# Performance work log

Measured on AMD Instinct MI355X. Metric: run time of the kernel, lower is better.

The kernel has to match this reference:

```python
import jax, jax.numpy as jnp
import numpy as np

EPS = 1e-6
B, S, D = 2, 2048, 2048
NH, NKV, HD = 16, 4, 128
DFF = 5632
WINDOW = 512


def rmsnorm(x, w):
    var = jnp.mean(x * x, axis=-1, keepdims=True)
    return x * jax.lax.rsqrt(var + EPS) * w


def rotate_half(x):
    x1, x2 = jnp.split(x, 2, axis=-1)
    return jnp.concatenate([-x2, x1], axis=-1)


def apply_rope(x, cos, sin):
    # x: (B, H, S, HD); cos/sin: (S, HD)
    return x * cos[None, None] + rotate_half(x) * sin[None, None]


def setup_inputs() -> dict:
    key = jax.random.key(0)
    ks = jax.random.split(key, 12)
    s = lambda n: (1.0 / np.sqrt(n))
    inp = {
        "hidden_states": jax.random.normal(ks[0], (B, S, D), jnp.float32),
        "cos": jnp.cos(jnp.arange(S)[:, None] / (10000.0 ** (jnp.concatenate([jnp.arange(HD // 2), jnp.arange(HD // 2)]) * 2.0 / HD))),
        "sin": jnp.sin(jnp.arange(S)[:, None] / (10000.0 ** (jnp.concatenate([jnp.arange(HD // 2), jnp.arange(HD // 2)]) * 2.0 / HD))),
        "ln1_w": jnp.ones((D,), jnp.float32),
        "ln2_w": jnp.ones((D,), jnp.float32),
        "wq": jax.random.normal(ks[1], (NH * HD, D), jnp.float32) * s(D),
        "wk": jax.random.normal(ks[2], (NKV * HD, D), jnp.float32) * s(D),
        "wv": jax.random.normal(ks[3], (NKV * HD, D), jnp.float32) * s(D),
        "wo": jax.random.normal(ks[4], (D, NH * HD), jnp.float32) * s(NH * HD),
        "w_gate": jax.random.normal(ks[5], (DFF, D), jnp.float32) * s(D),
        "w_up": jax.random.normal(ks[6], (DFF, D), jnp.float32) * s(D),
        "w_down": jax.random.normal(ks[7], (D, DFF), jnp.float32) * s(DFF),
    }
    return inp


def reference(hidden_states, cos, sin, ln1_w, ln2_w, wq, wk, wv, wo, w_gate, w_up, w_down):
    x = hidden_states
    # --- attention block ---
    h = rmsnorm(x, ln1_w)
    q = jnp.einsum("bsd,ed->bse", h, wq).reshape(B, S, NH, HD).transpose(0, 2, 1, 3)
    k = jnp.einsum("bsd,ed->bse", h, wk).reshape(B, S, NKV, HD).transpose(0, 2, 1, 3)
    v = jnp.einsum("bsd,ed->bse", h, wv).reshape(B, S, NKV, HD).transpose(0, 2, 1, 3)
    q = apply_rope(q, cos, sin)
    k = apply_rope(k, cos, sin)
    rep = NH // NKV
    k = jnp.repeat(k, rep, axis=1)  # (B, NH, S, HD)
    v = jnp.repeat(v, rep, axis=1)
    scale = 1.0 / np.sqrt(HD)
    scores = jnp.einsum("bhqd,bhkd->bhqk", q, k) * scale
    pos = jnp.arange(S)
    diff = pos[:, None] - pos[None, :]
    allowed = (diff >= 0) & (diff < WINDOW)  # causal + sliding window
    scores = jnp.where(allowed[None, None], scores, jnp.finfo(scores.dtype).min)
    attn = jax.nn.softmax(scores, axis=-1)
    out = jnp.einsum("bhqk,bhkd->bhqd", attn, v)
    out = out.transpose(0, 2, 1, 3).reshape(B, S, NH * HD)
    out = jnp.einsum("bse,de->bsd", out, wo)
    x = x + out
    # --- SwiGLU MLP block ---
    h = rmsnorm(x, ln2_w)
    gate = jax.nn.silu(jnp.einsum("bsd,fd->bsf", h, w_gate))
    up = jnp.einsum("bsd,fd->bsf", h, w_up)
    mlp = jnp.einsum("bsf,df->bsd", gate * up, w_down)
    return x + mlp
```

## Files before the change

kernel.cpp:

```cpp
#include <hip/hip_runtime.h>

typedef unsigned short u16;
typedef __attribute__((ext_vector_type(8))) short bf16x8;
typedef __attribute__((ext_vector_type(8))) unsigned short u16x8;
typedef __attribute__((ext_vector_type(4))) float f32x4;
typedef __attribute__((ext_vector_type(4))) _Float16 f16x4;

__device__ __forceinline__ u16 f2bf(float f) {
  union { float f; unsigned u; } v; v.f = f;
  unsigned r = v.u + 0x7fffu + ((v.u >> 16) & 1u);
  return (u16)(r >> 16);
}
__device__ __forceinline__ float bf2f(u16 u) {
  union { unsigned u; float f; } v; v.u = ((unsigned)u) << 16; return v.f;
}

#define GLOBAL_LOAD_LDS16(g, l)                                                \
  __builtin_amdgcn_global_load_lds(                                            \
      (const __attribute__((address_space(1))) void*)(g),                      \
      (__attribute__((address_space(3))) void*)(l), 16, 0, 0)

#define PHASE_TAIL()                                                           \
  asm volatile("s_waitcnt lgkmcnt(0)" ::: "memory");                           \
  __builtin_amdgcn_sched_barrier(0);                                           \
  __builtin_amdgcn_s_setprio(1)

__global__ __launch_bounds__(256) void rmsnorm_k(const float* __restrict__ x,
                                                 const float* __restrict__ w,
                                                 u16* __restrict__ out) {
  __shared__ float red[4];
  const int t = threadIdx.x;
  const size_t base = (size_t)blockIdx.x * 2048 + t * 8;
  float4 a = *(const float4*)(x + base);
  float4 b = *(const float4*)(x + base + 4);
  float ss = a.x * a.x + a.y * a.y + a.z * a.z + a.w * a.w +
             b.x * b.x + b.y * b.y + b.z * b.z + b.w * b.w;
#pragma unroll
  for (int o = 32; o; o >>= 1) ss += __shfl_xor(ss, o);
  if ((t & 63) == 0) red[t >> 6] = ss;
  __syncthreads();
  float rs = rsqrtf((red[0] + red[1] + red[2] + red[3]) * (1.0f / 2048.0f) + 1e-6f);
  float4 wa = *(const float4*)(w + t * 8);
  float4 wb = *(const float4*)(w + t * 8 + 4);
  u16x8 o8;
  o8[0] = f2bf(a.x * rs * wa.x); o8[1] = f2bf(a.y * rs * wa.y);
  o8[2] = f2bf(a.z * rs * wa.z); o8[3] = f2bf(a.w * rs * wa.w);
  o8[4] = f2bf(b.x * rs * wb.x); o8[5] = f2bf(b.y * rs * wb.y);
  o8[6] = f2bf(b.z * rs * wb.z); o8[7] = f2bf(b.w * rs * wb.w);
  *(u16x8*)(out + base) = o8;
}

__global__ __launch_bounds__(256) void rope_k(u16* __restrict__ buf,
                                              const float* __restrict__ cosp,
                                              const float* __restrict__ sinp,
                                              int nh, int total) {
  int i = blockIdx.x * 256 + threadIdx.x;
  if (i >= total) return;
  int d = i & 63;
  int hh = (i >> 6) % nh;
  int row = i / (64 * nh);
  int s = row & 2047;
  u16* p = buf + (size_t)row * (nh * 128) + hh * 128 + d;
  float x1 = bf2f(p[0]), x2 = bf2f(p[64]);
  float c1 = cosp[s * 128 + d], s1 = sinp[s * 128 + d];
  float c2 = cosp[s * 128 + d + 64], s2 = sinp[s * 128 + d + 64];
  p[0]  = f2bf(x1 * c1 - x2 * s1);
  p[64] = f2bf(x2 * c2 + x1 * s2);
}

__global__ __launch_bounds__(256) void rope_qkv(u16* __restrict__ buf,
                                                const float* __restrict__ cosp,
                                                const float* __restrict__ sinp) {
  int i = blockIdx.x * 256 + threadIdx.x;
  int d = i & 63;
  int hh = (i >> 6) % 20;
  int row = i / 1280;
  int s = row & 2047;
  int col = (hh < 16) ? hh * 128 + d : 2048 + (hh - 16) * 128 + d;
  u16* p = buf + (size_t)row * 3072 + col;
  float x1 = bf2f(p[0]), x2 = bf2f(p[64]);
  float c1 = cosp[s * 128 + d], s1 = sinp[s * 128 + d];
  float c2 = cosp[s * 128 + d + 64], s2 = sinp[s * 128 + d + 64];
  p[0]  = f2bf(x1 * c1 - x2 * s1);
  p[64] = f2bf(x2 * c2 + x1 * s2);
}

__global__ __launch_bounds__(256) void cvt_k(const float* __restrict__ s,
                                             u16* __restrict__ d, int n) {
  int stride = gridDim.x * 256 * 8;
  for (int i = (blockIdx.x * 256 + threadIdx.x) * 8; i < n; i += stride) {
    float4 a = *(const float4*)(s + i);
    float4 b = *(const float4*)(s + i + 4);
    u16x8 o;
    o[0] = f2bf(a.x); o[1] = f2bf(a.y); o[2] = f2bf(a.z); o[3] = f2bf(a.w);
    o[4] = f2bf(b.x); o[5] = f2bf(b.y); o[6] = f2bf(b.z); o[7] = f2bf(b.w);
    *(u16x8*)(d + i) = o;
  }
}

__global__ __launch_bounds__(256) void cvt3_k(const float* __restrict__ s0,
                                              const float* __restrict__ s1,
                                              const float* __restrict__ s2,
                                              u16* __restrict__ d,
                                              int n0, int n1, int n2) {
  int total = n0 + n1 + n2;
  int stride = gridDim.x * 256 * 8;
  for (int i = (blockIdx.x * 256 + threadIdx.x) * 8; i < total; i += stride) {
    const float* s; int off;
    if (i < n0)            { s = s0; off = i; }
    else if (i < n0 + n1)  { s = s1; off = i - n0; }
    else                   { s = s2; off = i - n0 - n1; }
    float4 a = *(const float4*)(s + off);
    float4 b = *(const float4*)(s + off + 4);
    u16x8 o;
    o[0] = f2bf(a.x); o[1] = f2bf(a.y); o[2] = f2bf(a.z); o[3] = f2bf(a.w);
    o[4] = f2bf(b.x); o[5] = f2bf(b.y); o[6] = f2bf(b.z); o[7] = f2bf(b.w);
    *(u16x8*)(d + i) = o;
  }
}

__device__ __forceinline__ void tile_swz(int bid, int nwg, int tm, int& bm, int& bn) {
  int cpx = nwg >> 3;
  int w = (bid & 7) * cpx + (bid >> 3);
  bm = w % tm;
  bn = w / tm;
}

template <int EPI>
__global__ __launch_bounds__(512, 2) void gemm2p(const u16* __restrict__ A,
                                                 const u16* __restrict__ Bw,
                                                 void* Cout, const float* resid,
                                                 int M, int N, int K) {
  const int NK = K >> 6;
  __shared__ u16 lds[73728];
  const int t = threadIdx.x, lane = t & 63, w = t >> 6;
  const int wm = w >> 2, wn = w & 3;
  const int l15 = lane & 15, lg = lane >> 4;
  int bm, bn;
  tile_swz(blockIdx.x, gridDim.x, M >> 7, bm, bn);

  const int r64 = t >> 3;
  const int gsrc = ((t & 7) ^ (r64 & 7)) * 8;
  const u16* Asrc[2];
#pragma unroll
  for (int u = 0; u < 2; ++u)
    Asrc[u] = A + (size_t)(bm * 128 + u * 64 + r64) * K + gsrc;
  const u16* Bsrc[4];
#pragma unroll
  for (int u = 0; u < 4; ++u)
    Bsrc[u] = Bw + (size_t)(bn * 256 + u * 64 + r64) * K + gsrc;
  const int d0 = t * 8;

#define STG_A2(buf, u, kt)                                                     \
  GLOBAL_LOAD_LDS16(Asrc[u] + (kt) * 64, &lds[(buf) * 24576 + (u) * 4096 + d0])
#define STG_B2(buf, u, kt)                                                     \
  GLOBAL_LOAD_LDS16(Bsrc[u] + (kt) * 64,                                       \
                    &lds[(buf) * 24576 + 8192 + (u) * 4096 + d0])

  const int swz0 = (lg ^ (l15 & 7)) * 8;
  const int swz1 = ((4 + lg) ^ (l15 & 7)) * 8;
  const int abase = wm * 4096 + l15 * 64;
  const int bbase = 8192 + wn * 4096 + l15 * 64;

  f32x4 acc[4][4] = {};
  bf16x8 af[4], bfr[4];

  STG_A2(0, 0, 0); STG_A2(0, 1, 0);
  STG_B2(0, 0, 0); STG_B2(0, 1, 0); STG_B2(0, 2, 0); STG_B2(0, 3, 0);
  STG_A2(1, 0, 1); STG_A2(1, 1, 1);
  STG_B2(1, 0, 1); STG_B2(1, 1, 1); STG_B2(1, 2, 1); STG_B2(1, 3, 1);
  asm volatile("s_waitcnt vmcnt(6)" ::: "memory");
  __builtin_amdgcn_s_barrier();

  for (int T = 0; T < NK; ++T) {
    const int bb = (T % 3) * 24576;
    const int nb = (T + 2) % 3;
#pragma unroll
    for (int i = 0; i < 4; ++i)
      af[i] = *(const bf16x8*)&lds[bb + abase + i * 1024 + swz0];
#pragma unroll
    for (int n = 0; n < 4; ++n)
      bfr[n] = *(const bf16x8*)&lds[bb + bbase + n * 1024 + swz0];
    if (T < NK - 2) { STG_A2(nb, 0, T + 2); STG_A2(nb, 1, T + 2); STG_B2(nb, 0, T + 2); }
    PHASE_TAIL();
#pragma unroll
    for (int i = 0; i < 4; ++i)
#pragma unroll
      for (int n = 0; n < 4; ++n)
        acc[i][n] = __builtin_amdgcn_mfma_f32_16x16x32_bf16(af[i], bfr[n], acc[i][n], 0, 0, 0);
    __builtin_amdgcn_s_setprio(0);
#pragma unroll
    for (int i = 0; i < 4; ++i)
      af[i] = *(const bf16x8*)&lds[bb + abase + i * 1024 + swz1];
#pragma unroll
    for (int n = 0; n < 4; ++n)
      bfr[n] = *(const bf16x8*)&lds[bb + bbase + n * 1024 + swz1];
    if (T < NK - 2) { STG_B2(nb, 1, T + 2); STG_B2(nb, 2, T + 2); STG_B2(nb, 3, T + 2); }
    PHASE_TAIL();
#pragma unroll
    for (int i = 0; i < 4; ++i)
#pragma unroll
      for (int n = 0; n < 4; ++n)
        acc[i][n] = __builtin_amdgcn_mfma_f32_16x16x32_bf16(af[i], bfr[n], acc[i][n], 0, 0, 0);
    __builtin_amdgcn_s_setprio(0);
    if (T < NK - 1) {
      if (T < NK - 2) asm volatile("s_waitcnt vmcnt(6)" ::: "memory");
      else            asm volatile("s_waitcnt vmcnt(0)" ::: "memory");
      __builtin_amdgcn_s_barrier();
    }
  }
#undef STG_A2
#undef STG_B2

#pragma unroll
  for (int mf = 0; mf < 4; ++mf)
#pragma unroll
    for (int nf = 0; nf < 4; ++nf)
#pragma unroll
      for (int r = 0; r < 4; ++r) {
        int row = bm * 128 + wm * 64 + mf * 16 + lg * 4 + r;
        int col = bn * 256 + wn * 64 + nf * 16 + l15;
        size_t idx = (size_t)row * N + col;
        if (EPI == 0)
          ((u16*)Cout)[idx] = f2bf(acc[mf][nf][r]);
        else
          ((float*)Cout)[idx] = resid[idx] + acc[mf][nf][r];
      }
}

__global__ __launch_bounds__(512, 2) void gateup2p(const u16* __restrict__ A,
                                                   const u16* __restrict__ Wg,
                                                   const u16* __restrict__ Wu,
                                                   u16* __restrict__ G) {
  constexpr int K = 2048, NK = 32;
  __shared__ u16 lds[73728];
  const int t = threadIdx.x, lane = t & 63, w = t >> 6;
  const int wm = w >> 2, wn = w & 3;
  const int l15 = lane & 15, lg = lane >> 4;
  int bm, bn;
  tile_swz(blockIdx.x, gridDim.x, 32, bm, bn);

  const int r64 = t >> 3;
  const int gsrc = ((t & 7) ^ (r64 & 7)) * 8;
  const u16* Asrc[2];
#pragma unroll
  for (int u = 0; u < 2; ++u)
    Asrc[u] = A + (size_t)(bm * 128 + u * 64 + r64) * K + gsrc;
  const u16* Wsel = (r64 < 32) ? Wg : Wu;
  const u16* Bsrc[4];
#pragma unroll
  for (int u = 0; u < 4; ++u)
    Bsrc[u] = Wsel + (size_t)(bn * 128 + u * 32 + (r64 & 31)) * K + gsrc;
  const int d0 = t * 8;

#define STG_A2(buf, u, kt)                                                     \
  GLOBAL_LOAD_LDS16(Asrc[u] + (kt) * 64, &lds[(buf) * 24576 + (u) * 4096 + d0])
#define STG_B2(buf, u, kt)                                                     \
  GLOBAL_LOAD_LDS16(Bsrc[u] + (kt) * 64,                                       \
                    &lds[(buf) * 24576 + 8192 + (u) * 4096 + d0])

  const int swz0 = (lg ^ (l15 & 7)) * 8;
  const int swz1 = ((4 + lg) ^ (l15 & 7)) * 8;
  const int abase = wm * 4096 + l15 * 64;
  const int bbase = 8192 + wn * 4096 + l15 * 64;

  f32x4 acc[4][4] = {};
  bf16x8 af[4], bfr[4];

  STG_A2(0, 0, 0); STG_A2(0, 1, 0);
  STG_B2(0, 0, 0); STG_B2(0, 1, 0); STG_B2(0, 2, 0); STG_B2(0, 3, 0);
  STG_A2(1, 0, 1); STG_A2(1, 1, 1);
  STG_B2(1, 0, 1); STG_B2(1, 1, 1); STG_B2(1, 2, 1); STG_B2(1, 3, 1);
  asm volatile("s_waitcnt vmcnt(6)" ::: "memory");
  __builtin_amdgcn_s_barrier();

  for (int T = 0; T < NK; ++T) {
    const int bb = (T % 3) * 24576;
    const int nb = (T + 2) % 3;
#pragma unroll
    for (int i = 0; i < 4; ++i)
      af[i] = *(const bf16x8*)&lds[bb + abase + i * 1024 + swz0];
#pragma unroll
    for (int n = 0; n < 4; ++n)
      bfr[n] = *(const bf16x8*)&lds[bb + bbase + n * 1024 + swz0];
    if (T < NK - 2) { STG_A2(nb, 0, T + 2); STG_A2(nb, 1, T + 2); STG_B2(nb, 0, T + 2); }
    PHASE_TAIL();
#pragma unroll
    for (int i = 0; i < 4; ++i)
#pragma unroll
      for (int n = 0; n < 4; ++n)
        acc[i][n] = __builtin_amdgcn_mfma_f32_16x16x32_bf16(af[i], bfr[n], acc[i][n], 0, 0, 0);
    __builtin_amdgcn_s_setprio(0);
#pragma unroll
    for (int i = 0; i < 4; ++i)
      af[i] = *(const bf16x8*)&lds[bb + abase + i * 1024 + swz1];
#pragma unroll
    for (int n = 0; n < 4; ++n)
      bfr[n] = *(const bf16x8*)&lds[bb + bbase + n * 1024 + swz1];
    if (T < NK - 2) { STG_B2(nb, 1, T + 2); STG_B2(nb, 2, T + 2); STG_B2(nb, 3, T + 2); }
    PHASE_TAIL();
#pragma unroll
    for (int i = 0; i < 4; ++i)
#pragma unroll
      for (int n = 0; n < 4; ++n)
        acc[i][n] = __builtin_amdgcn_mfma_f32_16x16x32_bf16(af[i], bfr[n], acc[i][n], 0, 0, 0);
    __builtin_amdgcn_s_setprio(0);
    if (T < NK - 1) {
      if (T < NK - 2) asm volatile("s_waitcnt vmcnt(6)" ::: "memory");
      else            asm volatile("s_waitcnt vmcnt(0)" ::: "memory");
      __builtin_amdgcn_s_barrier();
    }
  }
#undef STG_A2
#undef STG_B2

#pragma unroll
  for (int mf = 0; mf < 4; ++mf)
#pragma unroll
    for (int p = 0; p < 2; ++p)
#pragma unroll
      for (int r = 0; r < 4; ++r) {
        float gg = acc[mf][p][r], uu = acc[mf][p + 2][r];
        float sg = gg / (1.0f + __expf(-gg));
        int row = bm * 128 + wm * 64 + mf * 16 + lg * 4 + r;
        int col = bn * 128 + wn * 32 + p * 16 + l15;
        G[(size_t)row * 5632 + col] = f2bf(sg * uu);
      }
}

template <int EPI>
__global__ __launch_bounds__(256) void gemm_bt(const u16* __restrict__ A,
                                               const float* __restrict__ Bw,
                                               void* Cout, const float* resid,
                                               int M, int N, int K) {
  __shared__ u16 sA[128 * 32];
  __shared__ u16 sB[128 * 40];
  const int t = threadIdx.x, lane = t & 63, w = t >> 6;
  const int l15 = lane & 15, lg = lane >> 4;
  const int tn = N >> 7;
  const int bm = blockIdx.x / tn, bn = blockIdx.x % tn;
  const int wr = (w >> 1) << 6, wc = (w & 1) << 6;

  const u16* Ag  = A + (size_t)(bm * 128 + (t >> 2)) * K + (t & 3) * 8;
  const u16* Ag2 = Ag + (size_t)64 * K;
  const float* Bg  = Bw + (size_t)(bn * 128 + (t >> 2)) * K + (t & 3) * 8;
  const float* Bg2 = Bg + (size_t)64 * K;
  u16* sBp  = &sB[(t >> 2) * 40 + (t & 3) * 8];
  u16* sBp2 = sBp + 64 * 40;

  f32x4 acc[4][4] = {};

  for (int kt = 0; kt < K; kt += 32) {
    float4 b0 = *(const float4*)(Bg + kt);
    float4 b1 = *(const float4*)(Bg + kt + 4);
    float4 c0 = *(const float4*)(Bg2 + kt);
    float4 c1 = *(const float4*)(Bg2 + kt + 4);
    GLOBAL_LOAD_LDS16(Ag + kt, &sA[t * 8]);
    GLOBAL_LOAD_LDS16(Ag2 + kt, &sA[64 * 32 + t * 8]);
    u16x8 bs;
    bs[0] = f2bf(b0.x); bs[1] = f2bf(b0.y); bs[2] = f2bf(b0.z); bs[3] = f2bf(b0.w);
    bs[4] = f2bf(b1.x); bs[5] = f2bf(b1.y); bs[6] = f2bf(b1.z); bs[7] = f2bf(b1.w);
    *(u16x8*)sBp = bs;
    bs[0] = f2bf(c0.x); bs[1] = f2bf(c0.y); bs[2] = f2bf(c0.z); bs[3] = f2bf(c0.w);
    bs[4] = f2bf(c1.x); bs[5] = f2bf(c1.y); bs[6] = f2bf(c1.z); bs[7] = f2bf(c1.w);
    *(u16x8*)sBp2 = bs;
    __syncthreads();
    bf16x8 af[4], bfr[4];
#pragma unroll
    for (int m = 0; m < 4; ++m)
      af[m] = *(const bf16x8*)&sA[(wr + m * 16 + l15) * 32 + lg * 8];
#pragma unroll
    for (int n = 0; n < 4; ++n)
      bfr[n] = *(const bf16x8*)&sB[(wc + n * 16 + l15) * 40 + lg * 8];
#pragma unroll
    for (int m = 0; m < 4; ++m)
#pragma unroll
      for (int n = 0; n < 4; ++n)
        acc[m][n] = __builtin_amdgcn_mfma_f32_16x16x32_bf16(af[m], bfr[n], acc[m][n], 0, 0, 0);
    __syncthreads();
  }
#pragma unroll
  for (int m = 0; m < 4; ++m)
#pragma unroll
    for (int n = 0; n < 4; ++n)
#pragma unroll
      for (int r = 0; r < 4; ++r) {
        int row = bm * 128 + wr + m * 16 + lg * 4 + r;
        int col = bn * 128 + wc + n * 16 + l15;
        size_t idx = (size_t)row * N + col;
        if (EPI == 0)
          ((u16*)Cout)[idx] = f2bf(acc[m][n][r]);
        else
          ((float*)Cout)[idx] = resid[idx] + acc[m][n][r];
      }
}

__global__ __launch_bounds__(512) void gemm_gateup(const u16* __restrict__ A,
                                                   const float* __restrict__ Wg,
                                                   const float* __restrict__ Wu,
                                                   u16* __restrict__ G) {
  constexpr int N = 5632, K = 2048;
  __shared__ u16 sA[128 * 32];
  __shared__ u16 sB1[128 * 40];
  __shared__ u16 sB2[128 * 40];
  const int t = threadIdx.x, lane = t & 63, w = t >> 6;
  const int l15 = lane & 15, lg = lane >> 4;
  const int bm = blockIdx.x / 44, bn = blockIdx.x % 44;
  const int wr = (w >> 2) << 6, wc = (w & 3) << 5;

  const u16* Ag = A + (size_t)(bm * 128 + (t >> 2)) * K + (t & 3) * 8;
  const float* Bg1 = Wg + (size_t)(bn * 128 + (t >> 2)) * K + (t & 3) * 8;
  const float* Bg2 = Wu + (size_t)(bn * 128 + (t >> 2)) * K + (t & 3) * 8;
  const int sboff = (t >> 2) * 40 + (t & 3) * 8;

  f32x4 acc1[4][2] = {};
  f32x4 acc2[4][2] = {};

  for (int kt = 0; kt < K; kt += 32) {
    float4 g0 = *(const float4*)(Bg1 + kt);
    float4 g1 = *(const float4*)(Bg1 + kt + 4);
    float4 u0 = *(const float4*)(Bg2 + kt);
    float4 u1 = *(const float4*)(Bg2 + kt + 4);
    GLOBAL_LOAD_LDS16(Ag + kt, &sA[t * 8]);
    u16x8 bs;
    bs[0] = f2bf(g0.x); bs[1] = f2bf(g0.y); bs[2] = f2bf(g0.z); bs[3] = f2bf(g0.w);
    bs[4] = f2bf(g1.x); bs[5] = f2bf(g1.y); bs[6] = f2bf(g1.z); bs[7] = f2bf(g1.w);
    *(u16x8*)&sB1[sboff] = bs;
    bs[0] = f2bf(u0.x); bs[1] = f2bf(u0.y); bs[2] = f2bf(u0.z); bs[3] = f2bf(u0.w);
    bs[4] = f2bf(u1.x); bs[5] = f2bf(u1.y); bs[6] = f2bf(u1.z); bs[7] = f2bf(u1.w);
    *(u16x8*)&sB2[sboff] = bs;
    __syncthreads();
    bf16x8 af[4], b1f[2], b2f[2];
#pragma unroll
    for (int m = 0; m < 4; ++m)
      af[m] = *(const bf16x8*)&sA[(wr + m * 16 + l15) * 32 + lg * 8];
#pragma unroll
    for (int n = 0; n < 2; ++n) {
      b1f[n] = *(const bf16x8*)&sB1[(wc + n * 16 + l15) * 40 + lg * 8];
      b2f[n] = *(const bf16x8*)&sB2[(wc + n * 16 + l15) * 40 + lg * 8];
    }
#pragma unroll
    for (int m = 0; m < 4; ++m)
#pragma unroll
      for (int n = 0; n < 2; ++n) {
        acc1[m][n] = __builtin_amdgcn_mfma_f32_16x16x32_bf16(af[m], b1f[n], acc1[m][n], 0, 0, 0);
        acc2[m][n] = __builtin_amdgcn_mfma_f32_16x16x32_bf16(af[m], b2f[n], acc2[m][n], 0, 0, 0);
      }
    __syncthreads();
  }
#pragma unroll
  for (int m = 0; m < 4; ++m)
#pragma unroll
    for (int n = 0; n < 2; ++n)
#pragma unroll
      for (int r = 0; r < 4; ++r) {
        int row = bm * 128 + wr + m * 16 + lg * 4 + r;
        int col = bn * 128 + wc + n * 16 + l15;
        float ga = acc1[m][n][r], uu = acc2[m][n][r];
        float sg = ga / (1.0f + __expf(-ga));
        G[(size_t)row * N + col] = f2bf(sg * uu);
      }
}

__global__ __launch_bounds__(256) void attn_k(const u16* __restrict__ Q,
                                              const u16* __restrict__ K,
                                              const u16* __restrict__ V,
                                              u16* __restrict__ O,
                                              int qstr, int kvstr) {
  const int lane = threadIdx.x & 63;
  const int wid = blockIdx.x * 4 + (threadIdx.x >> 6);
  const int qt = wid & 127;
  const int h = (wid >> 7) & 15;
  const int b = wid >> 11;
  const int q0 = qt << 4;
  const int kvh = h >> 2;
  const int l15 = lane & 15, lg = lane >> 4;

  bf16x8 qf[4];
  {
    const u16* qp = Q + (size_t)((b << 11) + q0 + l15) * qstr + h * 128 + lg * 8;
#pragma unroll
    for (int ds = 0; ds < 4; ++ds) qf[ds] = *(const bf16x8*)(qp + ds * 32);
  }
  float m_run = -1e30f, l_run = 0.0f;
  f32x4 oacc[8];
#pragma unroll
  for (int db = 0; db < 8; ++db) oacc[db] = f32x4{0.f, 0.f, 0.f, 0.f};

  int lo = q0 - 511;
  if (lo < 0) lo = 0;
  for (int kb = (lo & ~15); kb <= q0; kb += 16) {
    f32x4 st = {0.f, 0.f, 0.f, 0.f};
    const u16* kp = K + (size_t)((b << 11) + kb + l15) * kvstr + kvh * 128 + lg * 8;
#pragma unroll
    for (int ds = 0; ds < 4; ++ds)
      st = __builtin_amdgcn_mfma_f32_16x16x32_bf16(*(const bf16x8*)(kp + ds * 32),
                                                   qf[ds], st, 0, 0, 0);
    const int qpos = q0 + l15;
    float pe[4];
    float tmax = -1e30f;
#pragma unroll
    for (int r = 0; r < 4; ++r) {
      int j = kb + lg * 4 + r;
      int d = qpos - j;
      bool ok = (d >= 0) && (d < 512);
      pe[r] = ok ? st[r] * 0.08838834764831845f : -1e30f;
      tmax = fmaxf(tmax, pe[r]);
    }
    tmax = fmaxf(tmax, __shfl_xor(tmax, 16));
    tmax = fmaxf(tmax, __shfl_xor(tmax, 32));
    float m_new = fmaxf(m_run, tmax);
    float corr = __expf(m_run - m_new);
    float psum = 0.0f;
#pragma unroll
    for (int r = 0; r < 4; ++r) {
      float e = (pe[r] > -1e29f) ? __expf(pe[r] - m_new) : 0.0f;
      pe[r] = e;
      psum += e;
    }
    psum += __shfl_xor(psum, 16);
    psum += __shfl_xor(psum, 32);
    l_run = l_run * corr + psum;
    m_run = m_new;

    f16x4 pf;
#pragma unroll
    for (int r = 0; r < 4; ++r) pf[r] = (_Float16)pe[r];

    float f0 = __shfl(corr, lg * 4 + 0);
    float f1 = __shfl(corr, lg * 4 + 1);
    float f2 = __shfl(corr, lg * 4 + 2);
    float f3 = __shfl(corr, lg * 4 + 3);
    const u16* vp = V + (size_t)((b << 11) + kb + lg * 4) * kvstr + kvh * 128 + l15;
#pragma unroll
    for (int db = 0; db < 8; ++db) {
      oacc[db][0] *= f0; oacc[db][1] *= f1; oacc[db][2] *= f2; oacc[db][3] *= f3;
      f16x4 vf;
#pragma unroll
      for (int e = 0; e < 4; ++e)
        vf[e] = (_Float16)bf2f(vp[(size_t)e * kvstr + db * 16]);
      oacc[db] = __builtin_amdgcn_mfma_f32_16x16x16f16(pf, vf, oacc[db], 0, 0, 0);
    }
  }
  float inv = 1.0f / l_run;
  float g0 = __shfl(inv, lg * 4 + 0);
  float g1 = __shfl(inv, lg * 4 + 1);
  float g2 = __shfl(inv, lg * 4 + 2);
  float g3 = __shfl(inv, lg * 4 + 3);
  u16* op = O + (size_t)((b << 11) + q0 + lg * 4) * 2048 + h * 128 + l15;
#pragma unroll
  for (int db = 0; db < 8; ++db) {
    op[0 * 2048 + db * 16] = f2bf(oacc[db][0] * g0);
    op[1 * 2048 + db * 16] = f2bf(oacc[db][1] * g1);
    op[2 * 2048 + db * 16] = f2bf(oacc[db][2] * g2);
    op[3 * 2048 + db * 16] = f2bf(oacc[db][3] * g3);
  }
}

extern "C" void kernel_launch(void* const* d_in, const int* in_sizes, int n_in,
                              void* d_out, int out_size, void* d_ws, size_t ws_size,
                              hipStream_t stream) {
  const float* x    = (const float*)d_in[0];
  const float* cosp = (const float*)d_in[1];
  const float* sinp = (const float*)d_in[2];
  const float* ln1  = (const float*)d_in[3];
  const float* ln2  = (const float*)d_in[4];
  const float* wq   = (const float*)d_in[5];
  const float* wk   = (const float*)d_in[6];
  const float* wv   = (const float*)d_in[7];
  const float* wo   = (const float*)d_in[8];
  const float* wg   = (const float*)d_in[9];
  const float* wu   = (const float*)d_in[10];
  const float* wd   = (const float*)d_in[11];
  float* out = (float*)d_out;

  const size_t SZ_HQ  = 8388608;
  const size_t SZ_KV  = 2097152;
  const size_t SZ_QKV = 12582912;
  const size_t SZ_G   = 23068672;
  const size_t SZ_WB  = 23068672;
  const size_t need_old = (SZ_HQ * 3 + SZ_KV * 2 + SZ_G) * 2;
  const size_t need_new = (SZ_HQ * 2 + SZ_QKV + SZ_G + SZ_WB) * 2;
  if (ws_size < need_old) return;

  if (ws_size >= need_new) {
    u16* h   = (u16*)d_ws;
    u16* qkv = h + SZ_HQ;
    u16* at  = qkv + SZ_QKV;
    u16* g   = at + SZ_HQ;
    u16* wb  = g + SZ_G;
    u16* wqb = wb;
    u16* wob = wb;
    u16* wgb = wb;
    u16* wdb = wb;

    rmsnorm_k<<<4096, 256, 0, stream>>>(x, ln1, h);
    cvt3_k<<<2048, 256, 0, stream>>>(wq, wk, wv, wqb, 4194304, 1048576, 1048576);
    gemm2p<0><<<384, 512, 0, stream>>>(h, wqb, qkv, nullptr, 4096, 3072, 2048);
    rope_qkv<<<20480, 256, 0, stream>>>(qkv, cosp, sinp);
    attn_k<<<1024, 256, 0, stream>>>(qkv, qkv + 2048, qkv + 2560, at, 3072, 3072);
    cvt_k<<<2048, 256, 0, stream>>>(wo, wob, 4194304);
    gemm2p<1><<<256, 512, 0, stream>>>(at, wob, d_out, x, 4096, 2048, 2048);
    rmsnorm_k<<<4096, 256, 0, stream>>>(out, ln2, h);
    cvt3_k<<<2048, 256, 0, stream>>>(wg, wu, wu, wgb, 11534336, 11534336, 0);
    gateup2p<<<1408, 512, 0, stream>>>(h, wgb, wgb + 11534336, g);
    cvt_k<<<2048, 256, 0, stream>>>(wd, wdb, 11534336);
    gemm2p<1><<<256, 512, 0, stream>>>(g, wdb, d_out, out, 4096, 2048, 5632);
  } else {
    u16* h  = (u16*)d_ws;
    u16* q  = h + SZ_HQ;
    u16* kk = q + SZ_HQ;
    u16* vv = kk + SZ_KV;
    u16* at = vv + SZ_KV;
    u16* g  = at + SZ_HQ;

    rmsnorm_k<<<4096, 256, 0, stream>>>(x, ln1, h);
    gemm_bt<0><<<512, 256, 0, stream>>>(h, wq, q,  nullptr, 4096, 2048, 2048);
    gemm_bt<0><<<128, 256, 0, stream>>>(h, wk, kk, nullptr, 4096, 512, 2048);
    gemm_bt<0><<<128, 256, 0, stream>>>(h, wv, vv, nullptr, 4096, 512, 2048);
    rope_k<<<16384, 256, 0, stream>>>(q, cosp, sinp, 16, 4194304);
    rope_k<<<4096, 256, 0, stream>>>(kk, cosp, sinp, 4, 1048576);
    attn_k<<<1024, 256, 0, stream>>>(q, kk, vv, at, 2048, 512);
    gemm_bt<1><<<512, 256, 0, stream>>>(at, wo, d_out, x, 4096, 2048, 2048);
    rmsnorm_k<<<4096, 256, 0, stream>>>(out, ln2, h);
    gemm_gateup<<<1408, 512, 0, stream>>>(h, wg, wu, g);
    gemm_bt<1><<<512, 256, 0, stream>>>(g, wd, d_out, out, 4096, 2048, 5632);
  }
}
```

Baseline: 586.1 us.

## Enlarge gate/up GEMM tile to 256 rows with thinner K steps

The fused gate/up SwiGLU GEMM is restructured so each block computes 256 rows by 128 interleaved gate/up columns instead of 128 by 128. K is now staged 32 elements at a time over 64 iterations with a triple-buffered LDS ring, and the swizzle changes to match. The block count halves. Each warp holds twice the accumulators, which raises arithmetic intensity and reduces re-reads of the weight tile. In exchange, register pressure rises and there are fewer blocks to fill the GPU.

```diff
diff --git a/kernel.cpp b/kernel.cpp
--- a/kernel.cpp
+++ b/kernel.cpp
@@ -228,62 +228,58 @@
       }
 }
 
-__global__ __launch_bounds__(512, 2) void gateup2p(const u16* __restrict__ A,
-                                                   const u16* __restrict__ Wg,
-                                                   const u16* __restrict__ Wu,
-                                                   u16* __restrict__ G) {
-  constexpr int K = 2048, NK = 32;
-  __shared__ u16 lds[73728];
+__global__ __launch_bounds__(512, 2) void gateupT(const u16* __restrict__ A,
+                                                  const u16* __restrict__ Wg,
+                                                  const u16* __restrict__ Wu,
+                                                  u16* __restrict__ G) {
+  constexpr int K = 2048, NK = 64;
+  __shared__ u16 lds[49152];
   const int t = threadIdx.x, lane = t & 63, w = t >> 6;
   const int wm = w >> 2, wn = w & 3;
   const int l15 = lane & 15, lg = lane >> 4;
   int bm, bn;
-  tile_swz(blockIdx.x, gridDim.x, 32, bm, bn);
-
-  const int r64 = t >> 3;
-  const int gsrc = ((t & 7) ^ (r64 & 7)) * 8;
+  tile_swz(blockIdx.x, gridDim.x, 16, bm, bn);
+
+  const int srow = t >> 2;
+  const int scol = ((t & 3) ^ ((t >> 3) & 3)) * 8;
   const u16* Asrc[2];
-#pragma unroll
-  for (int u = 0; u < 2; ++u)
-    Asrc[u] = A + (size_t)(bm * 128 + u * 64 + r64) * K + gsrc;
-  const u16* Wsel = (r64 < 32) ? Wg : Wu;
-  const u16* Bsrc[4];
-#pragma unroll
-  for (int u = 0; u < 4; ++u)
-    Bsrc[u] = Wsel + (size_t)(bn * 128 + u * 32 + (r64 & 31)) * K + gsrc;
+  Asrc[0] = A + (size_t)(bm * 256 + srow) * K + scol;
+  Asrc[1] = A + (size_t)(bm * 256 + 128 + srow) * K + scol;
+  const u16* Bsrc[2];
+  Bsrc[0] = Wg + (size_t)(bn * 128 + srow) * K + scol;
+  Bsrc[1] = Wu + (size_t)(bn * 128 + srow) * K + scol;
   const int d0 = t * 8;
 
-#define STG_A2(buf, u, kt)                                                     \
-  GLOBAL_LOAD_LDS16(Asrc[u] + (kt) * 64, &lds[(buf) * 24576 + (u) * 4096 + d0])
-#define STG_B2(buf, u, kt)                                                     \
-  GLOBAL_LOAD_LDS16(Bsrc[u] + (kt) * 64,                                       \
-                    &lds[(buf) * 24576 + 8192 + (u) * 4096 + d0])
-
-  const int swz0 = (lg ^ (l15 & 7)) * 8;
-  const int swz1 = ((4 + lg) ^ (l15 & 7)) * 8;
-  const int abase = wm * 4096 + l15 * 64;
-  const int bbase = 8192 + wn * 4096 + l15 * 64;
-
-  f32x4 acc[4][4] = {};
+#define STG_AT(buf, u, kt)                                                     \
+  GLOBAL_LOAD_LDS16(Asrc[u] + (kt) * 32, &lds[(buf) * 16384 + (u) * 4096 + d0])
+#define STG_BT(buf, u, kt)                                                     \
+  GLOBAL_LOAD_LDS16(Bsrc[u] + (kt) * 32,                                       \
+                    &lds[(buf) * 16384 + 8192 + (u) * 4096 + d0])
+
+  const int swz = (lg ^ ((l15 >> 1) & 3)) * 8;
+  const int abase = (wm * 128 + l15) * 32 + swz;
+  const int bbase = 8192 + (wn * 32 + l15) * 32 + swz;
+
+  f32x4 acc[8][4] = {};
   bf16x8 af[4], bfr[4];
 
-  STG_A2(0, 0, 0); STG_A2(0, 1, 0);
-  STG_B2(0, 0, 0); STG_B2(0, 1, 0); STG_B2(0, 2, 0); STG_B2(0, 3, 0);
-  STG_A2(1, 0, 1); STG_A2(1, 1, 1);
-  STG_B2(1, 0, 1); STG_B2(1, 1, 1); STG_B2(1, 2, 1); STG_B2(1, 3, 1);
-  asm volatile("s_waitcnt vmcnt(6)" ::: "memory");
+  STG_AT(0, 0, 0); STG_AT(0, 1, 0); STG_BT(0, 0, 0); STG_BT(0, 1, 0);
+  STG_AT(1, 0, 1); STG_AT(1, 1, 1); STG_BT(1, 0, 1); STG_BT(1, 1, 1);
+  asm volatile("s_waitcnt vmcnt(4)" ::: "memory");
   __builtin_amdgcn_s_barrier();
 
   for (int T = 0; T < NK; ++T) {
-    const int bb = (T % 3) * 24576;
+    const int bb = (T % 3) * 16384;
     const int nb = (T + 2) % 3;
 #pragma unroll
     for (int i = 0; i < 4; ++i)
-      af[i] = *(const bf16x8*)&lds[bb + abase + i * 1024 + swz0];
-#pragma unroll
-    for (int n = 0; n < 4; ++n)
-      bfr[n] = *(const bf16x8*)&lds[bb + bbase + n * 1024 + swz0];
-    if (T < NK - 2) { STG_A2(nb, 0, T + 2); STG_A2(nb, 1, T + 2); STG_B2(nb, 0, T + 2); }
+      af[i] = *(const bf16x8*)&lds[bb + abase + i * 512];
+#pragma unroll
+    for (int n = 0; n < 2; ++n) {
+      bfr[n]     = *(const bf16x8*)&lds[bb + bbase + n * 512];
+      bfr[2 + n] = *(const bf16x8*)&lds[bb + bbase + 4096 + n * 512];
+    }
+    if (T < NK - 2) { STG_AT(nb, 0, T + 2); STG_AT(nb, 1, T + 2); }
     PHASE_TAIL();
 #pragma unroll
     for (int i = 0; i < 4; ++i)
@@ -293,36 +289,33 @@
     __builtin_amdgcn_s_setprio(0);
 #pragma unroll
     for (int i = 0; i < 4; ++i)
-      af[i] = *(const bf16x8*)&lds[bb + abase + i * 1024 + swz1];
-#pragma unroll
-    for (int n = 0; n < 4; ++n)
-      bfr[n] = *(const bf16x8*)&lds[bb + bbase + n * 1024 + swz1];
-    if (T < NK - 2) { STG_B2(nb, 1, T + 2); STG_B2(nb, 2, T + 2); STG_B2(nb, 3, T + 2); }
+      af[i] = *(const bf16x8*)&lds[bb + abase + (4 + i) * 512];
+    if (T < NK - 2) { STG_BT(nb, 0, T + 2); STG_BT(nb, 1, T + 2); }
     PHASE_TAIL();
 #pragma unroll
     for (int i = 0; i < 4; ++i)
 #pragma unroll
       for (int n = 0; n < 4; ++n)
-        acc[i][n] = __builtin_amdgcn_mfma_f32_16x16x32_bf16(af[i], bfr[n], acc[i][n], 0, 0, 0);
+        acc[4 + i][n] = __builtin_amdgcn_mfma_f32_16x16x32_bf16(af[i], bfr[n], acc[4 + i][n], 0, 0, 0);
     __builtin_amdgcn_s_setprio(0);
     if (T < NK - 1) {
-      if (T < NK - 2) asm volatile("s_waitcnt vmcnt(6)" ::: "memory");
+      if (T < NK - 2) asm volatile("s_waitcnt vmcnt(4)" ::: "memory");
       else            asm volatile("s_waitcnt vmcnt(0)" ::: "memory");
       __builtin_amdgcn_s_barrier();
     }
   }
-#undef STG_A2
-#undef STG_B2
-
-#pragma unroll
-  for (int mf = 0; mf < 4; ++mf)
+#undef STG_AT
+#undef STG_BT
+
+#pragma unroll
+  for (int mf = 0; mf < 8; ++mf)
 #pragma unroll
     for (int p = 0; p < 2; ++p)
 #pragma unroll
       for (int r = 0; r < 4; ++r) {
         float gg = acc[mf][p][r], uu = acc[mf][p + 2][r];
         float sg = gg / (1.0f + __expf(-gg));
-        int row = bm * 128 + wm * 64 + mf * 16 + lg * 4 + r;
+        int row = bm * 256 + wm * 128 + mf * 16 + lg * 4 + r;
         int col = bn * 128 + wn * 32 + p * 16 + l15;
         G[(size_t)row * 5632 + col] = f2bf(sg * uu);
       }
@@ -603,7 +596,7 @@
     gemm2p<1><<<256, 512, 0, stream>>>(at, wob, d_out, x, 4096, 2048, 2048);
     rmsnorm_k<<<4096, 256, 0, stream>>>(out, ln2, h);
     cvt3_k<<<2048, 256, 0, stream>>>(wg, wu, wu, wgb, 11534336, 11534336, 0);
-    gateup2p<<<1408, 512, 0, stream>>>(h, wgb, wgb + 11534336, g);
+    gateupT<<<704, 512, 0, stream>>>(h, wgb, wgb + 11534336, g);
     cvt_k<<<2048, 256, 0, stream>>>(wd, wdb, 11534336);
     gemm2p<1><<<256, 512, 0, stream>>>(g, wdb, d_out, out, 4096, 2048, 5632);
   } else {
```

Measured after the change: 570.2 us. -2.7%, faster.
